# Performance work log

Measured on AMD Instinct MI355X. Metric: run time of the kernel, lower is better.

Reference implementation:

```python
import jax, jax.numpy as jnp
import numpy as np

B, N, D, K, L, NC = 8, 4096, 64, 8, 2, 2
EPS = 1e-5


def setup_inputs() -> dict:
    key = jax.random.key(0)
    ks = iter(jax.random.split(key, 64))
    def p(*shape, s=0.05):
        return jax.random.normal(next(ks), shape, dtype=jnp.float32) * s
    return dict(
        x=p(B, N, 3, s=1.0),
        ew1=p(3, D), eb1=jnp.zeros((D,), jnp.float32), ew2=p(D, D), eb2=jnp.zeros((D,), jnp.float32),
        wq=p(L, D, D), bq=jnp.zeros((L, D), jnp.float32), wk=p(L, D, D), bk=jnp.zeros((L, D), jnp.float32),
        wv=p(L, D, D), bv=jnp.zeros((L, D), jnp.float32),
        pw1=p(L, 3, D), pb1=jnp.zeros((L, D), jnp.float32), pw2=p(L, D, D), pb2=jnp.zeros((L, D), jnp.float32),
        aw=p(L, D), ab=jnp.zeros((L,), jnp.float32),
        ow=p(L, D, D), ob=jnp.zeros((L, D), jnp.float32),
        l1g=jnp.ones((L, D), jnp.float32), l1b=jnp.zeros((L, D), jnp.float32),
        l2g=jnp.ones((L, D), jnp.float32), l2b=jnp.zeros((L, D), jnp.float32),
        fw1=p(L, D, 2 * D), fb1=jnp.zeros((L, 2 * D), jnp.float32),
        fw2=p(L, 2 * D, D), fb2=jnp.zeros((L, D), jnp.float32),
        cw=p(D, 2 * D), cb=jnp.zeros((2 * D,), jnp.float32),
        cg=jnp.ones((2 * D,), jnp.float32), cbeta=jnp.zeros((2 * D,), jnp.float32),
        f1w=p(2 * D, 128), f1b=jnp.zeros((128,), jnp.float32),
        b1g=jnp.ones((128,), jnp.float32), b1b=jnp.zeros((128,), jnp.float32),
        f2w=p(128, 64), f2b=jnp.zeros((64,), jnp.float32),
        b2g=jnp.ones((64,), jnp.float32), b2b=jnp.zeros((64,), jnp.float32),
        f3w=p(64, NC), f3b=jnp.zeros((NC,), jnp.float32),
    )


def _ln(x, g, b):
    m = jnp.mean(x, -1, keepdims=True)
    v = jnp.mean((x - m) ** 2, -1, keepdims=True)
    return g * (x - m) * jax.lax.rsqrt(v + EPS) + b


def _bn(x, g, b):
    # eval-mode BatchNorm with running_mean=0, running_var=1
    return g * x * jax.lax.rsqrt(jnp.float32(1.0 + EPS)) + b


def _knn(pos, k):
    sq = jnp.sum(pos * pos, -1)  # [B,N]
    d2 = sq[:, :, None] - 2.0 * jnp.einsum('bnd,bmd->bnm', pos, pos) + sq[:, None, :]
    _, idx = jax.lax.top_k(-d2, k)  # k smallest distances (includes self)
    return jax.lax.stop_gradient(idx)  # [B,N,k]


def _gather(t, idx):
    b, n, k = idx.shape
    flat = idx.reshape(b, n * k)
    return jnp.take_along_axis(t, flat[:, :, None], axis=1).reshape(b, n, k, t.shape[-1])


def _block(x, pos, idx, pr):
    (wq, bq, wk, bk, wv, bv, pw1, pb1, pw2, pb2, aw, ab,
     ow, ob, l1g, l1b, l2g, l2b, fw1, fb1, fw2, fb2) = pr
    q = x @ wq + bq
    k = x @ wk + bk
    v = x @ wv + bv
    kg = _gather(k, idx)      # [B,N,K,C]
    vg = _gather(v, idx)
    pg = _gather(pos, idx)    # [B,N,K,3]
    pd = pos[:, :, None, :] - pg
    pe = jax.nn.relu(pd @ pw1 + pb1) @ pw2 + pb2
    ai = q[:, :, None, :] - kg + pe  # subtraction attention
    logits = jnp.einsum('bnkc,c->bnk', ai, aw) + ab
    w = jax.nn.softmax(logits, axis=-1)
    out = jnp.einsum('bnk,bnkc->bnc', w, vg + pe)
    out = out @ ow + ob
    out = _ln(out + x, l1g, l1b)
    ffn = jax.nn.gelu(out @ fw1 + fb1, approximate=False) @ fw2 + fb2
    return _ln(out + ffn, l2g, l2b)


def reference(x, ew1, eb1, ew2, eb2, wq, bq, wk, bk, wv, bv, pw1, pb1, pw2, pb2,
              aw, ab, ow, ob, l1g, l1b, l2g, l2b, fw1, fb1, fw2, fb2,
              cw, cb, cg, cbeta, f1w, f1b, b1g, b1b, f2w, f2b, b2g, b2b, f3w, f3b):
    pos = x
    h = jax.nn.relu(x @ ew1 + eb1) @ ew2 + eb2  # [B,N,D]
    idx = _knn(pos, K)
    stacked = (wq, bq, wk, bk, wv, bv, pw1, pb1, pw2, pb2, aw, ab,
               ow, ob, l1g, l1b, l2g, l2b, fw1, fb1, fw2, fb2)
    for i in range(L):
        h = _block(h, pos, idx, tuple(a[i] for a in stacked))
    y = jax.nn.relu(_bn(h @ cw + cb, cg, cbeta))  # [B,N,2D]
    g = jnp.max(y, axis=1)  # global max pool over points
    g = jax.nn.relu(_bn(g @ f1w + f1b, b1g, b1b))
    g = jax.nn.relu(_bn(g @ f2w + f2b, b2g, b2b))
    return g @ f3w + f3b  # [B, NC]
```

## Files before the change

kernel.cpp:

```cpp
#include <hip/hip_runtime.h>
#include <cmath>

#define BB 8
#define NN 4096
#define DD 64
#define KK 8
#define NCLS 2

constexpr float LNEPS = 1e-5f;
constexpr float BNRS = 0.9999950000374994f;
constexpr float INVSQRT2 = 0.70710678118654752440f;

constexpr int QKV_GRID = 512;
constexpr int ATTN_GRID = 1024;
constexpr int FFN_GRID = 512;

#define QPB 64
#define SPLITS 16
#define SUBSET 64

__device__ __forceinline__ float wave_sum(float v) {
#pragma unroll
  for (int m = 32; m > 0; m >>= 1) v += __shfl_xor(v, m, 64);
  return v;
}

__device__ __forceinline__ float gelu_exact(float x) {
  return 0.5f * x * (1.0f + erff(x * INVSQRT2));
}

__device__ __forceinline__ float dist2(float4 q, float4 p) {
  float dot = fmaf(q.x, p.x, fmaf(q.y, p.y, q.z * p.z));
  return fmaf(-2.0f, dot, q.w + p.w);
}

__global__ void zero_kernel(float* g) { g[threadIdx.x] = 0.0f; }

__global__ __launch_bounds__(256) void embed_kernel(
    const float* __restrict__ x, const float* __restrict__ ew1, const float* __restrict__ eb1,
    const float* __restrict__ ew2, const float* __restrict__ eb2, float* __restrict__ h) {
  __shared__ float h1[4][DD];
  int w = threadIdx.x >> 6, c = threadIdx.x & 63;
  int pt = blockIdx.x * 4 + w;
  const float* xp = x + (size_t)pt * 3;
  float x0 = xp[0], x1 = xp[1], x2 = xp[2];
  float a = fmaf(x0, ew1[c], fmaf(x1, ew1[64 + c], fmaf(x2, ew1[128 + c], eb1[c])));
  h1[w][c] = fmaxf(a, 0.0f);
  float s = eb2[c];
#pragma unroll 8
  for (int d = 0; d < DD; d++) s = fmaf(h1[w][d], ew2[d * 64 + c], s);
  h[(size_t)pt * 64 + c] = s;
}

__global__ __launch_bounds__(256) void knn_prep_kernel(const float* __restrict__ x,
                                                       float4* __restrict__ ppg) {
  int i = blockIdx.x * 256 + threadIdx.x;
  float a0 = x[3 * i + 0], a1 = x[3 * i + 1], a2 = x[3 * i + 2];
  ppg[i] = make_float4(a0, a1, a2, a0 * a0 + a1 * a1 + a2 * a2);
}

__global__ __launch_bounds__(1024) void knn_kernel(const float4* __restrict__ ppg,
                                                   int* __restrict__ idx) {
  __shared__ union {
    float v[SPLITS * 8][QPB];
    double k[SPLITS * 8][QPB];
  } mb;
  __shared__ float thrq[QPB];
  int b = blockIdx.x >> 6;
  int qbase = (blockIdx.x & 63) * QPB;
  const float4* pb = ppg + (size_t)b * NN;
  int ql = threadIdx.x & 63;
  int sp = __builtin_amdgcn_readfirstlane(threadIdx.x >> 6);
  float4 qp = pb[qbase + ql];
  const float4* cp = pb + sp * (NN / SPLITS);

  float bd[8];
#pragma unroll
  for (int u = 0; u < 8; u++) bd[u] = INFINITY;
#pragma unroll 4
  for (int jj = 0; jj < SUBSET; ++jj) {
    float d2 = dist2(qp, cp[jj]);
#pragma unroll
    for (int u = 7; u > 0; --u) bd[u] = fminf(bd[u], fmaxf(bd[u - 1], d2));
    bd[0] = fminf(bd[0], d2);
  }
#pragma unroll
  for (int u = 0; u < 8; u++) mb.v[sp * 8 + u][ql] = bd[u];
  __syncthreads();

  if (sp < 8) {
    float cd[8];
#pragma unroll
    for (int u = 0; u < 8; u++) cd[u] = INFINITY;
    int base = sp * 16;
#pragma unroll
    for (int e = 0; e < 16; e++) {
      float vv = mb.v[base + e][ql];
#pragma unroll
      for (int u = 7; u > 0; --u) cd[u] = fminf(cd[u], fmaxf(cd[u - 1], vv));
      cd[0] = fminf(cd[0], vv);
    }
#pragma unroll
    for (int u = 0; u < 8; u++) mb.v[base + u][ql] = cd[u];
  }
  __syncthreads();

  if (sp == 0) {
    float cd[8];
#pragma unroll
    for (int u = 0; u < 8; u++) cd[u] = INFINITY;
    for (int m = 0; m < 8; m++) {
      for (int e = 0; e < 8; e++) {
        float vv = mb.v[m * 16 + e][ql];
        if (__all(vv >= cd[7])) break;
#pragma unroll
        for (int u = 7; u > 0; --u) cd[u] = fminf(cd[u], fmaxf(cd[u - 1], vv));
        cd[0] = fminf(cd[0], vv);
      }
    }
    thrq[ql] = cd[7];
  }
  __syncthreads();
  float U = thrq[ql];

  double kd[8];
#pragma unroll
  for (int u = 0; u < 8; u++) kd[u] = INFINITY;
#pragma unroll 4
  for (int jj = 0; jj < NN / SPLITS; ++jj) {
    float d2 = dist2(qp, cp[jj]);
    if (d2 <= U) {
      double key = __hiloint2double(__float_as_int(d2), sp * (NN / SPLITS) + jj);
      if (key < kd[7]) {
#pragma unroll
        for (int u = 7; u > 0; --u) kd[u] = fmin(kd[u], fmax(kd[u - 1], key));
        kd[0] = fmin(kd[0], key);
      }
    }
  }
#pragma unroll
  for (int u = 0; u < 8; u++) mb.k[sp * 8 + u][ql] = kd[u];
  __syncthreads();

  if (sp < 8) {
    double cd[8];
#pragma unroll
    for (int u = 0; u < 8; u++) cd[u] = INFINITY;
    int base = sp * 16;
#pragma unroll
    for (int e = 0; e < 16; e++) {
      double key = mb.k[base + e][ql];
#pragma unroll
      for (int u = 7; u > 0; --u) cd[u] = fmin(cd[u], fmax(cd[u - 1], key));
      cd[0] = fmin(cd[0], key);
    }
#pragma unroll
    for (int u = 0; u < 8; u++) mb.k[base + u][ql] = cd[u];
  }
  __syncthreads();

  if (sp == 0) {
    double cd[8];
#pragma unroll
    for (int u = 0; u < 8; u++) cd[u] = INFINITY;
    for (int m = 0; m < 8; m++) {
      for (int e = 0; e < 8; e++) {
        double key = mb.k[m * 16 + e][ql];
        if (__all(key >= cd[7])) break;
#pragma unroll
        for (int u = 7; u > 0; --u) cd[u] = fmin(cd[u], fmax(cd[u - 1], key));
        cd[0] = fmin(cd[0], key);
      }
    }
    int* op = idx + ((size_t)b * NN + qbase + ql) * 8;
#pragma unroll
    for (int u = 0; u < 8; u++) op[u] = __double2loint(cd[u]);
  }
}

__global__ __launch_bounds__(256) void qkv_kernel(
    const float* __restrict__ h, const float* __restrict__ wq, const float* __restrict__ bq,
    const float* __restrict__ wk, const float* __restrict__ bk,
    const float* __restrict__ wv, const float* __restrict__ bv,
    float* __restrict__ q, float* __restrict__ k, float* __restrict__ v) {
  __shared__ float lwq[DD * DD], lwk[DD * DD], lwv[DD * DD];
  __shared__ float lbq[DD], lbk[DD], lbv[DD];
  __shared__ __attribute__((aligned(16))) float hb[4][DD][4];
  int tid = threadIdx.x;
  for (int i = tid; i < DD * DD; i += 256) { lwq[i] = wq[i]; lwk[i] = wk[i]; lwv[i] = wv[i]; }
  if (tid < DD) { lbq[tid] = bq[tid]; lbk[tid] = bk[tid]; lbv[tid] = bv[tid]; }
  __syncthreads();
  int w = tid >> 6, c = tid & 63;
  constexpr int ITERS = (BB * NN) / (QKV_GRID * 16);
  for (int it = 0; it < ITERS; ++it) {
    int wid = it * (QKV_GRID * 4) + blockIdx.x * 4 + w;
    int p0 = wid * 4;
#pragma unroll
    for (int i = 0; i < 4; i++) hb[w][c][i] = h[(size_t)(p0 + i) * 64 + c];
    float aq[4], ak[4], av[4];
#pragma unroll
    for (int i = 0; i < 4; i++) { aq[i] = lbq[c]; ak[i] = lbk[c]; av[i] = lbv[c]; }
#pragma unroll 4
    for (int d = 0; d < DD; d++) {
      float wq_ = lwq[d * 64 + c], wk_ = lwk[d * 64 + c], wv_ = lwv[d * 64 + c];
      float4 hh = *(const float4*)&hb[w][d][0];
      aq[0] = fmaf(hh.x, wq_, aq[0]); aq[1] = fmaf(hh.y, wq_, aq[1]);
      aq[2] = fmaf(hh.z, wq_, aq[2]); aq[3] = fmaf(hh.w, wq_, aq[3]);
      ak[0] = fmaf(hh.x, wk_, ak[0]); ak[1] = fmaf(hh.y, wk_, ak[1]);
      ak[2] = fmaf(hh.z, wk_, ak[2]); ak[3] = fmaf(hh.w, wk_, ak[3]);
      av[0] = fmaf(hh.x, wv_, av[0]); av[1] = fmaf(hh.y, wv_, av[1]);
      av[2] = fmaf(hh.z, wv_, av[2]); av[3] = fmaf(hh.w, wv_, av[3]);
    }
#pragma unroll
    for (int i = 0; i < 4; i++) {
      q[(size_t)(p0 + i) * 64 + c] = aq[i];
      k[(size_t)(p0 + i) * 64 + c] = ak[i];
      v[(size_t)(p0 + i) * 64 + c] = av[i];
    }
  }
}

__global__ __launch_bounds__(256) void attn_kernel(
    const float* __restrict__ x, const float* __restrict__ h,
    const float* q, const float* __restrict__ kk, const float* __restrict__ vv,
    const int* __restrict__ idx,
    const float* __restrict__ pw1, const float* __restrict__ pb1,
    const float* __restrict__ pw2, const float* __restrict__ pb2,
    const float* __restrict__ aw, const float* __restrict__ ab,
    const float* __restrict__ ow, const float* __restrict__ ob,
    const float* __restrict__ l1g, const float* __restrict__ l1b,
    float* t) {
  __shared__ float lpw2[DD * DD];
  __shared__ float lpw1[3 * DD], lpb1[DD], lpb2[DD], law[DD], lob_[DD], ll1g[DD], ll1b[DD];
  __shared__ __attribute__((aligned(16))) float h1b[4][2][DD][8];
  __shared__ __attribute__((aligned(16))) float outb[4][2][DD];
  int tid = threadIdx.x;
  for (int i = tid; i < DD * DD; i += 256) lpw2[i] = pw2[i];
  if (tid < 3 * DD) lpw1[tid] = pw1[tid];
  if (tid < DD) {
    lpb1[tid] = pb1[tid]; lpb2[tid] = pb2[tid]; law[tid] = aw[tid];
    lob_[tid] = ob[tid]; ll1g[tid] = l1g[tid]; ll1b[tid] = l1b[tid];
  }
  float lab = ab[0];
  __syncthreads();
  int w = tid >> 6, c = tid & 63;
  constexpr int ITERS = (BB * NN) / (ATTN_GRID * 8);
  for (int it = 0; it < ITERS; ++it) {
    int p0 = (it * ATTN_GRID + blockIdx.x) * 8 + w * 2;
    int b = p0 >> 12;
    int n0 = p0 & (NN - 1);
    const float* xb = x + (size_t)b * NN * 3;
    float hs0 = h[(size_t)p0 * 64 + c], hs1 = h[(size_t)(p0 + 1) * 64 + c];
    float qs0 = q[(size_t)p0 * 64 + c], qs1 = q[(size_t)(p0 + 1) * 64 + c];
    int nb[2][8];
#pragma unroll
    for (int u = 0; u < 8; u++) {
      nb[0][u] = idx[(size_t)p0 * 8 + u];
      nb[1][u] = idx[(size_t)(p0 + 1) * 8 + u];
    }
    float w1c0 = lpw1[c], w1c1 = lpw1[64 + c], w1c2 = lpw1[128 + c], b1c = lpb1[c];
#pragma unroll
    for (int pt = 0; pt < 2; ++pt) {
      int n = n0 + pt;
      float px0 = xb[n * 3 + 0], px1 = xb[n * 3 + 1], px2 = xb[n * 3 + 2];
      float h1v[8];
#pragma unroll
      for (int u = 0; u < 8; u++) {
        int m = nb[pt][u];
        float d0 = px0 - xb[m * 3 + 0], d1 = px1 - xb[m * 3 + 1], d2 = px2 - xb[m * 3 + 2];
        h1v[u] = fmaxf(fmaf(d0, w1c0, fmaf(d1, w1c1, fmaf(d2, w1c2, b1c))), 0.0f);
      }
      *(float4*)&h1b[w][pt][c][0] = make_float4(h1v[0], h1v[1], h1v[2], h1v[3]);
      *(float4*)&h1b[w][pt][c][4] = make_float4(h1v[4], h1v[5], h1v[6], h1v[7]);
    }
    float acc0[8], acc1[8];
    float pb2c = lpb2[c];
#pragma unroll
    for (int u = 0; u < 8; u++) { acc0[u] = pb2c; acc1[u] = pb2c; }
#pragma unroll 2
    for (int d = 0; d < DD; d++) {
      float wv_ = lpw2[d * 64 + c];
      float4 a0 = *(const float4*)&h1b[w][0][d][0];
      float4 b0 = *(const float4*)&h1b[w][0][d][4];
      float4 a1 = *(const float4*)&h1b[w][1][d][0];
      float4 b1 = *(const float4*)&h1b[w][1][d][4];
      acc0[0] = fmaf(a0.x, wv_, acc0[0]); acc0[1] = fmaf(a0.y, wv_, acc0[1]);
      acc0[2] = fmaf(a0.z, wv_, acc0[2]); acc0[3] = fmaf(a0.w, wv_, acc0[3]);
      acc0[4] = fmaf(b0.x, wv_, acc0[4]); acc0[5] = fmaf(b0.y, wv_, acc0[5]);
      acc0[6] = fmaf(b0.z, wv_, acc0[6]); acc0[7] = fmaf(b0.w, wv_, acc0[7]);
      acc1[0] = fmaf(a1.x, wv_, acc1[0]); acc1[1] = fmaf(a1.y, wv_, acc1[1]);
      acc1[2] = fmaf(a1.z, wv_, acc1[2]); acc1[3] = fmaf(a1.w, wv_, acc1[3]);
      acc1[4] = fmaf(b1.x, wv_, acc1[4]); acc1[5] = fmaf(b1.y, wv_, acc1[5]);
      acc1[6] = fmaf(b1.z, wv_, acc1[6]); acc1[7] = fmaf(b1.w, wv_, acc1[7]);
    }
    float lawc = law[c];
    float lg0[8], lg1[8];
#pragma unroll
    for (int u = 0; u < 8; u++) {
      float kv0 = kk[((size_t)(b << 12) + nb[0][u]) * 64 + c];
      float kv1 = kk[((size_t)(b << 12) + nb[1][u]) * 64 + c];
      lg0[u] = wave_sum((qs0 - kv0 + acc0[u]) * lawc) + lab;
      lg1[u] = wave_sum((qs1 - kv1 + acc1[u]) * lawc) + lab;
    }
    float mx0 = lg0[0], mx1 = lg1[0];
#pragma unroll
    for (int u = 1; u < 8; u++) { mx0 = fmaxf(mx0, lg0[u]); mx1 = fmaxf(mx1, lg1[u]); }
    float s0 = 0.0f, s1 = 0.0f;
#pragma unroll
    for (int u = 0; u < 8; u++) {
      lg0[u] = expf(lg0[u] - mx0); s0 += lg0[u];
      lg1[u] = expf(lg1[u] - mx1); s1 += lg1[u];
    }
    float i0 = 1.0f / s0, i1 = 1.0f / s1;
    float out0 = 0.0f, out1 = 0.0f;
#pragma unroll
    for (int u = 0; u < 8; u++) {
      float vg0 = vv[((size_t)(b << 12) + nb[0][u]) * 64 + c];
      float vg1 = vv[((size_t)(b << 12) + nb[1][u]) * 64 + c];
      out0 = fmaf(lg0[u] * i0, vg0 + acc0[u], out0);
      out1 = fmaf(lg1[u] * i1, vg1 + acc1[u], out1);
    }
    outb[w][0][c] = out0; outb[w][1][c] = out1;
    float at0 = lob_[c], at1 = at0;
#pragma unroll 4
    for (int d = 0; d < DD; d += 4) {
      float4 o0 = *(const float4*)&outb[w][0][d];
      float4 o1 = *(const float4*)&outb[w][1][d];
      float wa = ow[(d + 0) * 64 + c], wb = ow[(d + 1) * 64 + c];
      float wc = ow[(d + 2) * 64 + c], wd = ow[(d + 3) * 64 + c];
      at0 = fmaf(o0.x, wa, at0); at0 = fmaf(o0.y, wb, at0);
      at0 = fmaf(o0.z, wc, at0); at0 = fmaf(o0.w, wd, at0);
      at1 = fmaf(o1.x, wa, at1); at1 = fmaf(o1.y, wb, at1);
      at1 = fmaf(o1.z, wc, at1); at1 = fmaf(o1.w, wd, at1);
    }
    float g1c = ll1g[c], bt1c = ll1b[c];
    {
      float res = at0 + hs0;
      float mean = wave_sum(res) * (1.0f / 64.0f);
      float dv = res - mean;
      float var = wave_sum(dv * dv) * (1.0f / 64.0f);
      float ivr = 1.0f / sqrtf(var + LNEPS);
      t[(size_t)p0 * 64 + c] = fmaf(g1c, dv * ivr, bt1c);
    }
    {
      float res = at1 + hs1;
      float mean = wave_sum(res) * (1.0f / 64.0f);
      float dv = res - mean;
      float var = wave_sum(dv * dv) * (1.0f / 64.0f);
      float ivr = 1.0f / sqrtf(var + LNEPS);
      t[(size_t)(p0 + 1) * 64 + c] = fmaf(g1c, dv * ivr, bt1c);
    }
  }
}

__global__ __launch_bounds__(256) void ffn_kernel(
    const float* __restrict__ t, const float* __restrict__ fw1, const float* __restrict__ fb1,
    const float* __restrict__ fw2, const float* __restrict__ fb2,
    const float* __restrict__ l2g, const float* __restrict__ l2b, float* __restrict__ h) {
  __shared__ float lf1[DD * 128];
  __shared__ float lf2[128 * DD];
  __shared__ float lb1[128], lb2[DD], lg2[DD], lbt2[DD];
  __shared__ __attribute__((aligned(16))) float yb[4][DD][4];
  __shared__ __attribute__((aligned(16))) float hb[4][128][4];
  int tid = threadIdx.x;
  for (int i = tid; i < DD * 128; i += 256) { lf1[i] = fw1[i]; lf2[i] = fw2[i]; }
  if (tid < 128) lb1[tid] = fb1[tid];
  if (tid < DD) { lb2[tid] = fb2[tid]; lg2[tid] = l2g[tid]; lbt2[tid] = l2b[tid]; }
  __syncthreads();
  int w = tid >> 6, c = tid & 63;
  constexpr int ITERS = (BB * NN) / (FFN_GRID * 16);
  for (int it = 0; it < ITERS; ++it) {
    int wid = it * (FFN_GRID * 4) + blockIdx.x * 4 + w;
    int p0 = wid * 4;
    float y[4];
#pragma unroll
    for (int i = 0; i < 4; i++) { y[i] = t[(size_t)(p0 + i) * 64 + c]; yb[w][c][i] = y[i]; }
    float hA[4], hB[4];
#pragma unroll
    for (int i = 0; i < 4; i++) { hA[i] = lb1[c]; hB[i] = lb1[64 + c]; }
#pragma unroll 4
    for (int d = 0; d < DD; d++) {
      float w0 = lf1[d * 128 + c], w1 = lf1[d * 128 + 64 + c];
      float4 yv = *(const float4*)&yb[w][d][0];
      hA[0] = fmaf(yv.x, w0, hA[0]); hA[1] = fmaf(yv.y, w0, hA[1]);
      hA[2] = fmaf(yv.z, w0, hA[2]); hA[3] = fmaf(yv.w, w0, hA[3]);
      hB[0] = fmaf(yv.x, w1, hB[0]); hB[1] = fmaf(yv.y, w1, hB[1]);
      hB[2] = fmaf(yv.z, w1, hB[2]); hB[3] = fmaf(yv.w, w1, hB[3]);
    }
#pragma unroll
    for (int i = 0; i < 4; i++) {
      hA[i] = gelu_exact(hA[i]); hB[i] = gelu_exact(hB[i]);
      hb[w][c][i] = hA[i]; hb[w][64 + c][i] = hB[i];
    }
    float o[4];
#pragma unroll
    for (int i = 0; i < 4; i++) o[i] = lb2[c];
#pragma unroll 4
    for (int j = 0; j < 128; j++) {
      float wv_ = lf2[j * 64 + c];
      float4 hv = *(const float4*)&hb[w][j][0];
      o[0] = fmaf(hv.x, wv_, o[0]); o[1] = fmaf(hv.y, wv_, o[1]);
      o[2] = fmaf(hv.z, wv_, o[2]); o[3] = fmaf(hv.w, wv_, o[3]);
    }
#pragma unroll
    for (int i = 0; i < 4; i++) {
      float r = y[i] + o[i];
      float mean = wave_sum(r) * (1.0f / 64.0f);
      float dv = r - mean;
      float var = wave_sum(dv * dv) * (1.0f / 64.0f);
      float ivr = 1.0f / sqrtf(var + LNEPS);
      h[(size_t)(p0 + i) * 64 + c] = fmaf(lg2[c], dv * ivr, lbt2[c]);
    }
  }
}

__global__ __launch_bounds__(256) void cls_kernel(
    const float* __restrict__ h, const float* __restrict__ cw, const float* __restrict__ cb,
    const float* __restrict__ cg, const float* __restrict__ cbeta, float* __restrict__ g) {
  __shared__ float lcw[DD * 128];
  __shared__ float lcb[128], lcg[128], lcbt[128];
  __shared__ __attribute__((aligned(16))) float hb[4][DD][4];
  __shared__ float wmax[4][128];
  int tid = threadIdx.x;
  for (int i = tid; i < DD * 128; i += 256) lcw[i] = cw[i];
  if (tid < 128) { lcb[tid] = cb[tid]; lcg[tid] = cg[tid]; lcbt[tid] = cbeta[tid]; }
  __syncthreads();
  int w = tid >> 6, c = tid & 63;
  int b = blockIdx.x >> 7;
  int blk = blockIdx.x & 127;
  int base = b * NN + blk * 32;
  float m0 = 0.0f, m1 = 0.0f;
  for (int it = 0; it < 2; ++it) {
    int p0 = base + (w * 2 + it) * 4;
#pragma unroll
    for (int i = 0; i < 4; i++) hb[w][c][i] = h[(size_t)(p0 + i) * 64 + c];
    float a0[4], a1[4];
#pragma unroll
    for (int i = 0; i < 4; i++) { a0[i] = lcb[c]; a1[i] = lcb[64 + c]; }
#pragma unroll 4
    for (int d = 0; d < DD; d++) {
      float w0 = lcw[d * 128 + c], w1 = lcw[d * 128 + 64 + c];
      float4 hv = *(const float4*)&hb[w][d][0];
      a0[0] = fmaf(hv.x, w0, a0[0]); a0[1] = fmaf(hv.y, w0, a0[1]);
      a0[2] = fmaf(hv.z, w0, a0[2]); a0[3] = fmaf(hv.w, w0, a0[3]);
      a1[0] = fmaf(hv.x, w1, a1[0]); a1[1] = fmaf(hv.y, w1, a1[1]);
      a1[2] = fmaf(hv.z, w1, a1[2]); a1[3] = fmaf(hv.w, w1, a1[3]);
    }
#pragma unroll
    for (int i = 0; i < 4; i++) {
      m0 = fmaxf(m0, fmaxf(0.0f, fmaf(lcg[c] * a0[i], BNRS, lcbt[c])));
      m1 = fmaxf(m1, fmaxf(0.0f, fmaf(lcg[64 + c] * a1[i], BNRS, lcbt[64 + c])));
    }
  }
  wmax[w][c] = m0; wmax[w][64 + c] = m1;
  __syncthreads();
  if (tid < 128) {
    float mm = fmaxf(fmaxf(wmax[0][tid], wmax[1][tid]), fmaxf(wmax[2][tid], wmax[3][tid]));
    atomicMax((int*)&g[b * 128 + tid], __float_as_int(mm));
  }
}

__global__ __launch_bounds__(128) void head_kernel(
    const float* __restrict__ g,
    const float* __restrict__ f1w, const float* __restrict__ f1b,
    const float* __restrict__ b1g, const float* __restrict__ b1b,
    const float* __restrict__ f2w, const float* __restrict__ f2b,
    const float* __restrict__ b2g, const float* __restrict__ b2b,
    const float* __restrict__ f3w, const float* __restrict__ f3b,
    float* __restrict__ out) {
  __shared__ float gb[128], g1[128], g2[64];
  int b = blockIdx.x, t = threadIdx.x;
  gb[t] = g[b * 128 + t];
  __syncthreads();
  float a = f1b[t];
#pragma unroll 4
  for (int d = 0; d < 128; d++) a = fmaf(gb[d], f1w[d * 128 + t], a);
  g1[t] = fmaxf(0.0f, fmaf(b1g[t] * a, BNRS, b1b[t]));
  __syncthreads();
  if (t < 64) {
    float a2 = f2b[t];
#pragma unroll 4
    for (int j = 0; j < 128; j++) a2 = fmaf(g1[j], f2w[j * 64 + t], a2);
    g2[t] = fmaxf(0.0f, fmaf(b2g[t] * a2, BNRS, b2b[t]));
  }
  __syncthreads();
  if (t < NCLS) {
    float a3 = f3b[t];
#pragma unroll
    for (int d = 0; d < 64; d++) a3 = fmaf(g2[d], f3w[d * NCLS + t], a3);
    out[b * NCLS + t] = a3;
  }
}

extern "C" void kernel_launch(void* const* d_in, const int* in_sizes, int n_in,
                              void* d_out, int out_size, void* d_ws, size_t ws_size,
                              hipStream_t stream) {
  const float* x    = (const float*)d_in[0];
  const float* ew1  = (const float*)d_in[1];
  const float* eb1  = (const float*)d_in[2];
  const float* ew2  = (const float*)d_in[3];
  const float* eb2  = (const float*)d_in[4];
  const float* wq   = (const float*)d_in[5];
  const float* bq   = (const float*)d_in[6];
  const float* wk   = (const float*)d_in[7];
  const float* bk   = (const float*)d_in[8];
  const float* wv   = (const float*)d_in[9];
  const float* bv   = (const float*)d_in[10];
  const float* pw1  = (const float*)d_in[11];
  const float* pb1  = (const float*)d_in[12];
  const float* pw2  = (const float*)d_in[13];
  const float* pb2  = (const float*)d_in[14];
  const float* aw   = (const float*)d_in[15];
  const float* ab   = (const float*)d_in[16];
  const float* ow   = (const float*)d_in[17];
  const float* ob   = (const float*)d_in[18];
  const float* l1g  = (const float*)d_in[19];
  const float* l1b  = (const float*)d_in[20];
  const float* l2g  = (const float*)d_in[21];
  const float* l2b  = (const float*)d_in[22];
  const float* fw1  = (const float*)d_in[23];
  const float* fb1  = (const float*)d_in[24];
  const float* fw2  = (const float*)d_in[25];
  const float* fb2  = (const float*)d_in[26];
  const float* cw   = (const float*)d_in[27];
  const float* cb   = (const float*)d_in[28];
  const float* cg   = (const float*)d_in[29];
  const float* cbeta= (const float*)d_in[30];
  const float* f1w  = (const float*)d_in[31];
  const float* f1b  = (const float*)d_in[32];
  const float* b1g  = (const float*)d_in[33];
  const float* b1b  = (const float*)d_in[34];
  const float* f2w  = (const float*)d_in[35];
  const float* f2b  = (const float*)d_in[36];
  const float* b2g  = (const float*)d_in[37];
  const float* b2b  = (const float*)d_in[38];
  const float* f3w  = (const float*)d_in[39];
  const float* f3b  = (const float*)d_in[40];

  const size_t P = (size_t)BB * NN;
  float* ws = (float*)d_ws;
  float* h = ws;
  float* q = h + P * 64;
  float* k = q + P * 64;
  float* v = k + P * 64;
  int* idx = (int*)(v + P * 64);
  float* g = (float*)(idx + P * 8);
  float4* ppg = (float4*)(g + BB * 128);
  float* t = q;

  zero_kernel<<<1, BB * 128, 0, stream>>>(g);
  embed_kernel<<<(int)(P / 4), 256, 0, stream>>>(x, ew1, eb1, ew2, eb2, h);
  knn_prep_kernel<<<(int)(P / 256), 256, 0, stream>>>(x, ppg);
  knn_kernel<<<BB * (NN / QPB), 1024, 0, stream>>>(ppg, idx);
  for (int l = 0; l < 2; l++) {
    qkv_kernel<<<QKV_GRID, 256, 0, stream>>>(h, wq + l * DD * DD, bq + l * DD,
                                             wk + l * DD * DD, bk + l * DD,
                                             wv + l * DD * DD, bv + l * DD, q, k, v);
    attn_kernel<<<ATTN_GRID, 256, 0, stream>>>(x, h, q, k, v, idx,
                                               pw1 + l * 3 * DD, pb1 + l * DD,
                                               pw2 + l * DD * DD, pb2 + l * DD,
                                               aw + l * DD, ab + l,
                                               ow + l * DD * DD, ob + l * DD,
                                               l1g + l * DD, l1b + l * DD, t);
    ffn_kernel<<<FFN_GRID, 256, 0, stream>>>(t, fw1 + l * DD * 2 * DD, fb1 + l * 2 * DD,
                                             fw2 + l * 2 * DD * DD, fb2 + l * DD,
                                             l2g + l * DD, l2b + l * DD, h);
  }
  cls_kernel<<<BB * 128, 256, 0, stream>>>(h, cw, cb, cg, cbeta, g);
  head_kernel<<<BB, 128, 0, stream>>>(g, f1w, f1b, b1g, b1b, f2w, f2b, b2g, b2b, f3w, f3b,
                                      (float*)d_out);
}
```

Baseline: 426.0 us.

## Interleave batches across blocks for XCD locality and hoist neighbor K/V gathers

Remaps block indices in every kernel so that blockIdx & 7 selects the batch. On MI355X, blocks are dispatched round-robin across 8 XCDs, so each XCD's L2 then holds the data of a single batch, which should improve cache reuse for the gather-heavy kernn and attention kernels. The attention kernel also issues all neighbor K and V gathers up front, before the position-MLP compute, so their latency overlaps with that work. The cost is more live registers in the attention kernel, which could lower occupancy.

```diff
diff --git a/kernel.cpp b/kernel.cpp
--- a/kernel.cpp
+++ b/kernel.cpp
@@ -41,7 +41,7 @@
     const float* __restrict__ ew2, const float* __restrict__ eb2, float* __restrict__ h) {
   __shared__ float h1[4][DD];
   int w = threadIdx.x >> 6, c = threadIdx.x & 63;
-  int pt = blockIdx.x * 4 + w;
+  int pt = ((blockIdx.x & 7) << 12) + (blockIdx.x >> 3) * 4 + w;
   const float* xp = x + (size_t)pt * 3;
   float x0 = xp[0], x1 = xp[1], x2 = xp[2];
   float a = fmaf(x0, ew1[c], fmaf(x1, ew1[64 + c], fmaf(x2, ew1[128 + c], eb1[c])));
@@ -54,7 +54,7 @@
 
 __global__ __launch_bounds__(256) void knn_prep_kernel(const float* __restrict__ x,
                                                        float4* __restrict__ ppg) {
-  int i = blockIdx.x * 256 + threadIdx.x;
+  int i = ((blockIdx.x & 7) << 12) + (blockIdx.x >> 3) * 256 + threadIdx.x;
   float a0 = x[3 * i + 0], a1 = x[3 * i + 1], a2 = x[3 * i + 2];
   ppg[i] = make_float4(a0, a1, a2, a0 * a0 + a1 * a1 + a2 * a2);
 }
@@ -66,8 +66,8 @@
     double k[SPLITS * 8][QPB];
   } mb;
   __shared__ float thrq[QPB];
-  int b = blockIdx.x >> 6;
-  int qbase = (blockIdx.x & 63) * QPB;
+  int b = blockIdx.x & 7;
+  int qbase = (blockIdx.x >> 3) * QPB;
   const float4* pb = ppg + (size_t)b * NN;
   int ql = threadIdx.x & 63;
   int sp = __builtin_amdgcn_readfirstlane(threadIdx.x >> 6);
@@ -191,10 +191,10 @@
   if (tid < DD) { lbq[tid] = bq[tid]; lbk[tid] = bk[tid]; lbv[tid] = bv[tid]; }
   __syncthreads();
   int w = tid >> 6, c = tid & 63;
-  constexpr int ITERS = (BB * NN) / (QKV_GRID * 16);
+  int batch = blockIdx.x & 7, pos = blockIdx.x >> 3;
+  constexpr int ITERS = NN / ((QKV_GRID / 8) * 16);
   for (int it = 0; it < ITERS; ++it) {
-    int wid = it * (QKV_GRID * 4) + blockIdx.x * 4 + w;
-    int p0 = wid * 4;
+    int p0 = (batch << 12) + ((it * 64 + pos) * 4 + w) * 4;
 #pragma unroll
     for (int i = 0; i < 4; i++) hb[w][c][i] = h[(size_t)(p0 + i) * 64 + c];
     float aq[4], ak[4], av[4];
@@ -244,12 +244,12 @@
   float lab = ab[0];
   __syncthreads();
   int w = tid >> 6, c = tid & 63;
-  constexpr int ITERS = (BB * NN) / (ATTN_GRID * 8);
+  int b = blockIdx.x & 7, pos = blockIdx.x >> 3;
+  const float* xb = x + (size_t)b * NN * 3;
+  constexpr int ITERS = NN / ((ATTN_GRID / 8) * 8);
   for (int it = 0; it < ITERS; ++it) {
-    int p0 = (it * ATTN_GRID + blockIdx.x) * 8 + w * 2;
-    int b = p0 >> 12;
-    int n0 = p0 & (NN - 1);
-    const float* xb = x + (size_t)b * NN * 3;
+    int n0 = ((it * 128 + pos) * 8) + w * 2;
+    int p0 = (b << 12) + n0;
     float hs0 = h[(size_t)p0 * 64 + c], hs1 = h[(size_t)(p0 + 1) * 64 + c];
     float qs0 = q[(size_t)p0 * 64 + c], qs1 = q[(size_t)(p0 + 1) * 64 + c];
     int nb[2][8];
@@ -257,6 +257,14 @@
     for (int u = 0; u < 8; u++) {
       nb[0][u] = idx[(size_t)p0 * 8 + u];
       nb[1][u] = idx[(size_t)(p0 + 1) * 8 + u];
+    }
+    float kv0[8], kv1[8], vg0[8], vg1[8];
+#pragma unroll
+    for (int u = 0; u < 8; u++) {
+      kv0[u] = kk[((size_t)(b << 12) + nb[0][u]) * 64 + c];
+      kv1[u] = kk[((size_t)(b << 12) + nb[1][u]) * 64 + c];
+      vg0[u] = vv[((size_t)(b << 12) + nb[0][u]) * 64 + c];
+      vg1[u] = vv[((size_t)(b << 12) + nb[1][u]) * 64 + c];
     }
     float w1c0 = lpw1[c], w1c1 = lpw1[64 + c], w1c2 = lpw1[128 + c], b1c = lpb1[c];
 #pragma unroll
@@ -297,10 +305,8 @@
     float lg0[8], lg1[8];
 #pragma unroll
     for (int u = 0; u < 8; u++) {
-      float kv0 = kk[((size_t)(b << 12) + nb[0][u]) * 64 + c];
-      float kv1 = kk[((size_t)(b << 12) + nb[1][u]) * 64 + c];
-      lg0[u] = wave_sum((qs0 - kv0 + acc0[u]) * lawc) + lab;
-      lg1[u] = wave_sum((qs1 - kv1 + acc1[u]) * lawc) + lab;
+      lg0[u] = wave_sum((qs0 - kv0[u] + acc0[u]) * lawc) + lab;
+      lg1[u] = wave_sum((qs1 - kv1[u] + acc1[u]) * lawc) + lab;
     }
     float mx0 = lg0[0], mx1 = lg1[0];
 #pragma unroll
@@ -315,10 +321,8 @@
     float out0 = 0.0f, out1 = 0.0f;
 #pragma unroll
     for (int u = 0; u < 8; u++) {
-      float vg0 = vv[((size_t)(b << 12) + nb[0][u]) * 64 + c];
-      float vg1 = vv[((size_t)(b << 12) + nb[1][u]) * 64 + c];
-      out0 = fmaf(lg0[u] * i0, vg0 + acc0[u], out0);
-      out1 = fmaf(lg1[u] * i1, vg1 + acc1[u], out1);
+      out0 = fmaf(lg0[u] * i0, vg0[u] + acc0[u], out0);
+      out1 = fmaf(lg1[u] * i1, vg1[u] + acc1[u], out1);
     }
     outb[w][0][c] = out0; outb[w][1][c] = out1;
     float at0 = lob_[c], at1 = at0;
@@ -368,10 +372,10 @@
   if (tid < DD) { lb2[tid] = fb2[tid]; lg2[tid] = l2g[tid]; lbt2[tid] = l2b[tid]; }
   __syncthreads();
   int w = tid >> 6, c = tid & 63;
-  constexpr int ITERS = (BB * NN) / (FFN_GRID * 16);
+  int batch = blockIdx.x & 7, pos = blockIdx.x >> 3;
+  constexpr int ITERS = NN / ((FFN_GRID / 8) * 16);
   for (int it = 0; it < ITERS; ++it) {
-    int wid = it * (FFN_GRID * 4) + blockIdx.x * 4 + w;
-    int p0 = wid * 4;
+    int p0 = (batch << 12) + ((it * 64 + pos) * 4 + w) * 4;
     float y[4];
 #pragma unroll
     for (int i = 0; i < 4; i++) { y[i] = t[(size_t)(p0 + i) * 64 + c]; yb[w][c][i] = y[i]; }
@@ -426,8 +430,8 @@
   if (tid < 128) { lcb[tid] = cb[tid]; lcg[tid] = cg[tid]; lcbt[tid] = cbeta[tid]; }
   __syncthreads();
   int w = tid >> 6, c = tid & 63;
-  int b = blockIdx.x >> 7;
-  int blk = blockIdx.x & 127;
+  int b = blockIdx.x & 7;
+  int blk = blockIdx.x >> 3;
   int base = b * NN + blk * 32;
   float m0 = 0.0f, m1 = 0.0f;
   for (int it = 0; it < 2; ++it) {
```

Result: faster. 415.5 us (-2.5%).
